# Kernel tuning notes

Hardware: AMD Instinct MI355X
Metric: run time of the kernel (lower is better)

## Reference

```python
import jax, jax.numpy as jnp
import numpy as np

VOCAB, EMBED, ZCH = 4096, 128, 256
B, H, W = 32, 16, 16


def setup_inputs() -> dict:
    key = jax.random.key(0)
    k1, k2, k3, k4 = jax.random.split(key, 4)
    z_e = jax.random.normal(k1, (B, ZCH, H, W), dtype=jnp.float32)
    pre_w = jax.random.normal(k2, (EMBED, ZCH), dtype=jnp.float32) * 0.02
    pre_b = jnp.zeros((EMBED,), dtype=jnp.float32)
    # codebook initialized uniform(-1/vocab, 1/vocab) like the torch module
    emb = jax.random.uniform(k3, (VOCAB, EMBED), dtype=jnp.float32,
                             minval=-1.0 / VOCAB, maxval=1.0 / VOCAB)
    post_w = jax.random.normal(k4, (ZCH, EMBED), dtype=jnp.float32) * 0.02
    post_b = jnp.zeros((ZCH,), dtype=jnp.float32)
    return {"z_e": z_e, "pre_w": pre_w, "pre_b": pre_b, "emb": emb,
            "post_w": post_w, "post_b": post_b}


def reference(z_e, pre_w, pre_b, emb, post_w, post_b):
    # pre_quant_conv: 1x1 conv == per-pixel linear, z_channels -> embed_dim
    z = jnp.einsum('bchw,ec->behw', z_e, pre_w) + pre_b[None, :, None, None]
    b, e, h, w = z.shape
    zf = z.transpose(0, 2, 3, 1).reshape(-1, e)                 # (b*h*w, e)
    # squared distance to all codebook vectors: |z|^2 + |c|^2 - 2 z.c
    dist = (jnp.sum(zf * zf, axis=1, keepdims=True)
            + jnp.sum(emb * emb, axis=1)
            - 2.0 * zf @ emb.T)                                  # (b*h*w, vocab)
    tokens = jnp.argmin(dist, axis=-1)                           # (b*h*w,)
    z_q = emb[tokens].reshape(b, h, w, e).transpose(0, 3, 1, 2)  # (b,e,h,w)
    # straight-through estimator
    dec_in = z + jax.lax.stop_gradient(z_q - z)
    # post_quant_conv: 1x1 conv embed_dim -> z_channels (decoder input)
    rec = jnp.einsum('behw,ce->bchw', dec_in, post_w) + post_b[None, :, None, None]
    return z, z_q, rec
```

## Files before the change

### kernel.cpp

```cpp
#include <hip/hip_runtime.h>
#include <hip/hip_bf16.h>
#include <cstdint>

#define NB   32
#define NC   256
#define NE   128
#define NS   256
#define NV   4096
#define NP   8192
#define NSPLIT 8

typedef unsigned short ushort_t;
typedef __attribute__((ext_vector_type(8))) short bf16x8;
typedef __attribute__((ext_vector_type(8))) unsigned short us8;
typedef __attribute__((ext_vector_type(4))) float f32x4;

__device__ __forceinline__ float bf2f(ushort_t u) {
    union { unsigned int i; float f; } x; x.i = ((unsigned int)u) << 16; return x.f;
}
__device__ __forceinline__ ushort_t f2bf(float f) {
    __hip_bfloat16 h = __float2bfloat16(f);
    ushort_t u; __builtin_memcpy(&u, &h, 2); return u;
}
__device__ __forceinline__ unsigned asu(float f) { unsigned u; __builtin_memcpy(&u,&f,4); return u; }
__device__ __forceinline__ float    asf(unsigned u) { float f; __builtin_memcpy(&f,&u,4); return f; }

__global__ __launch_bounds__(256) void pre_conv_pack(
    const float* __restrict__ z_e, const float* __restrict__ pre_w,
    const float* __restrict__ pre_b, const float* __restrict__ emb,
    float* __restrict__ out_z, ushort_t* __restrict__ Bpack,
    float* __restrict__ cnorm)
{
    __shared__ __align__(16) float wtile[16 * 256];
    __shared__ __align__(16) float part[4 * 16 * 64];

    const int t = threadIdx.x;

    if (blockIdx.x == 8) {
        const int v     = (blockIdx.y * 4 + blockIdx.z) * 32 + (t >> 3);
        const int chunk = t & 7;
        const float4* rp = (const float4*)(emb + (size_t)v * NE + chunk * 16);
        float4 x0 = rp[0], x1 = rp[1], x2 = rp[2], x3 = rp[3];
        float xs[16] = { x0.x, x0.y, x0.z, x0.w, x1.x, x1.y, x1.z, x1.w,
                         x2.x, x2.y, x2.z, x2.w, x3.x, x3.y, x3.z, x3.w };
        us8 h0, h1;
        float nn = 0.f;
#pragma unroll
        for (int j = 0; j < 8; j++) {
            nn = fmaf(xs[j], xs[j], nn);
            h0[j] = f2bf(xs[j]);
        }
#pragma unroll
        for (int j = 0; j < 8; j++) {
            nn = fmaf(xs[8 + j], xs[8 + j], nn);
            h1[j] = f2bf(xs[8 + j]);
        }
        nn += __shfl_xor(nn, 1);
        nn += __shfl_xor(nn, 2);
        nn += __shfl_xor(nn, 4);
        if (chunk == 0) cnorm[v] = 0.5f * nn;

        const int G  = v >> 4;
        const int ks = chunk >> 1;
        const int q0 = (chunk & 1) * 2;
        const int L0 = (v & 15) | (q0 << 4);
        const int L1 = (v & 15) | ((q0 + 1) << 4);
        *(us8*)(Bpack + ((size_t)G * 4 + ks) * 512 + L0 * 8) = h0;
        *(us8*)(Bpack + ((size_t)G * 4 + ks) * 512 + L1 * 8) = h1;
        return;
    }

    const int e0 = blockIdx.x * 16;
    const int b  = blockIdx.y;
    const int s0 = blockIdx.z * 64;

    for (int idx = t; idx < 16 * 256; idx += 256)
        wtile[idx] = pre_w[(e0 + (idx >> 8)) * 256 + (idx & 255)];
    __syncthreads();

    const int kq = t >> 6, sl = t & 63;
    float acc[16];
#pragma unroll
    for (int r = 0; r < 16; r++) acc[r] = 0.f;

    const float* zin = z_e + (size_t)(b * NC + kq * 64) * NS + s0 + sl;
    const int cb = kq * 64;
#pragma unroll 4
    for (int i = 0; i < 16; i++) {
        const int c = i * 4;
        float z0 = zin[(c + 0) * NS];
        float z1 = zin[(c + 1) * NS];
        float z2 = zin[(c + 2) * NS];
        float z3 = zin[(c + 3) * NS];
#pragma unroll
        for (int r = 0; r < 16; r++) {
            float4 w = *(const float4*)&wtile[r * 256 + cb + c];
            acc[r] = fmaf(z0, w.x, fmaf(z1, w.y, fmaf(z2, w.z, fmaf(z3, w.w, acc[r]))));
        }
    }
#pragma unroll
    for (int r = 0; r < 16; r++)
        part[(kq * 16 + r) * 64 + sl] = acc[r];
    __syncthreads();

    const int r4 = t >> 6, sl2 = t & 63;
#pragma unroll
    for (int j = 0; j < 4; j++) {
        const int r = j * 4 + r4;
        float v = pre_b[e0 + r]
                + part[(0 * 16 + r) * 64 + sl2]
                + part[(1 * 16 + r) * 64 + sl2]
                + part[(2 * 16 + r) * 64 + sl2]
                + part[(3 * 16 + r) * 64 + sl2];
        out_z[(size_t)(b * NE + e0 + r) * NS + s0 + sl2] = v;
    }
}

__global__ __launch_bounds__(256, 3) void score_mfma(
    const float* __restrict__ z, const ushort_t* __restrict__ Bpack,
    const float* __restrict__ cnorm, int* __restrict__ pidx4)
{
    __shared__ __align__(16) char smraw[37376];
    float* As  = (float*)smraw;
    float* r1  = (float*)smraw;
    float* r2  = (float*)(smraw + 16640);
    float* t4b = (float*)(smraw + 33280);

    const int t = threadIdx.x;
    const int wave = t >> 6, lane = t & 63;
    const int set = blockIdx.x;
    const int split = blockIdx.y;
    const int p0 = set * 64;
    const int b  = p0 >> 8;
    const int s0 = p0 & 255;

    for (int idx = t; idx < 64 * 128; idx += 256) {
        int k = idx >> 6, i = idx & 63;
        As[i * 132 + k] = z[(size_t)(b * NE + k) * NS + s0 + i];
    }
    __syncthreads();

    const int am = lane & 15, aq = lane >> 4;
    bf16x8 ah[4][4];
#pragma unroll
    for (int mt = 0; mt < 4; mt++)
#pragma unroll
        for (int ks = 0; ks < 4; ks++) {
            const unsigned* src = (const unsigned*)(As + (mt * 16 + am) * 132 + ks * 32 + aq * 8);
            union { unsigned u[4]; bf16x8 v; } pk;
#pragma unroll
            for (int pr = 0; pr < 4; pr++)
                pk.u[pr] = (src[2 * pr + 1] & 0xFFFF0000u) | (src[2 * pr] >> 16);
            ah[mt][ks] = pk.v;
        }
    __syncthreads();

    const int Gbase = split * 32 + wave * 8;
    float cn[8];
#pragma unroll
    for (int cgi = 0; cgi < 8; cgi++)
        cn[cgi] = cnorm[(Gbase + cgi) * 16 + am];

    float b1v[16], b2v[16];
#pragma unroll
    for (int i = 0; i < 16; i++) { b1v[i] = -1e30f; b2v[i] = -1e30f; }

    for (int cgi = 0; cgi < 8; cgi++) {
        const int G = Gbase + cgi;
        bf16x8 bh[4];
#pragma unroll
        for (int ks = 0; ks < 4; ks++)
            bh[ks] = *(const bf16x8*)(Bpack + ((size_t)G * 4 + ks) * 512 + lane * 8);

        f32x4 acc[4];
#pragma unroll
        for (int mt = 0; mt < 4; mt++) acc[mt] = (f32x4){0.f, 0.f, 0.f, 0.f};
#pragma unroll
        for (int ks = 0; ks < 4; ks++)
#pragma unroll
            for (int mt = 0; mt < 4; mt++)
                acc[mt] = __builtin_amdgcn_mfma_f32_16x16x32_bf16(ah[mt][ks], bh[ks], acc[mt], 0, 0, 0);

#pragma unroll
        for (int mt = 0; mt < 4; mt++)
#pragma unroll
            for (int reg = 0; reg < 4; reg++) {
                const int si = mt * 4 + reg;
                float sc = acc[mt][reg] - cn[cgi];
                float ev = asf((asu(sc) & ~7u) | (unsigned)cgi);
                b2v[si] = fmaxf(b2v[si], fminf(ev, b1v[si]));
                b1v[si] = fmaxf(b1v[si], ev);
            }
    }

    const int slot = wave * 16 + am;
#pragma unroll
    for (int mt = 0; mt < 4; mt++)
#pragma unroll
        for (int reg = 0; reg < 4; reg++) {
            int px = mt * 16 + aq * 4 + reg;
            r1[slot * 65 + px] = b1v[mt * 4 + reg];
            r2[slot * 65 + px] = b2v[mt * 4 + reg];
        }
    __syncthreads();

    {
        const int px = t >> 2, ch = t & 3;
        float t1 = -1e30f, t2 = -1e30f, t3 = -1e30f, t4 = -1e30f;
        for (int i = 0; i < 16; i++) {
            int sl = ch * 16 + i;
#pragma unroll
            for (int e = 0; e < 2; e++) {
                float raw = e ? r2[sl * 65 + px] : r1[sl * 65 + px];
                unsigned vb = asu(raw);
                float v = asf((vb & ~511u) | ((unsigned)sl << 3) | (vb & 7u));
                t4 = fmaxf(t4, fminf(v, t3));
                t3 = fmaxf(t3, fminf(v, t2));
                t2 = fmaxf(t2, fminf(v, t1));
                t1 = fmaxf(t1, v);
            }
        }
        float* dst = t4b + (px * 4 + ch) * 4;
        dst[0] = t1; dst[1] = t2; dst[2] = t3; dst[3] = t4;
    }
    __syncthreads();

    if (t < 64) {
        float u1 = -1e30f, u2 = -1e30f, u3 = -1e30f, u4 = -1e30f;
        for (int ch = 0; ch < 4; ch++) {
#pragma unroll
            for (int j = 0; j < 4; j++) {
                float v = t4b[(t * 4 + ch) * 4 + j];
                u4 = fmaxf(u4, fminf(v, u3));
                u3 = fmaxf(u3, fminf(v, u2));
                u2 = fmaxf(u2, fminf(v, u1));
                u1 = fmaxf(u1, v);
            }
        }
        const int p = p0 + t;
        float uu[4] = { u1, u2, u3, u4 };
#pragma unroll
        for (int j = 0; j < 4; j++) {
            unsigned bits = asu(uu[j]) & 511u;
            int w = (int)(bits >> 7), res = (int)((bits >> 3) & 15u), cg = (int)(bits & 7u);
            pidx4[((size_t)split * NP + p) * 4 + j] = split * 512 + (w * 8 + cg) * 16 + res;
        }
    }
}

__global__ __launch_bounds__(256) void rescore_gather(
    const float* __restrict__ z, const float* __restrict__ emb,
    const float* __restrict__ cnorm, const int* __restrict__ pidx4,
    float* __restrict__ out_zq)
{
    __shared__ __align__(16) float zl[16 * 132];
    __shared__ float bsl[16 * 16];
    __shared__ int   bil[16 * 16];
    __shared__ int   tok[16];

    const int t  = threadIdx.x;
    const int p0 = blockIdx.x * 16;
    const int b  = p0 >> 8;
    const int s0 = p0 & 255;

    for (int idx = t; idx < 16 * 128; idx += 256) {
        int k = idx >> 4, i = idx & 15;
        zl[i * 132 + k] = z[(size_t)(b * NE + k) * NS + s0 + i];
    }
    __syncthreads();

    const int il = t >> 4;
    const int cc = t & 15;
    const int p  = p0 + il;
    float bs = -1e30f; int bi = 0x7fffffff;
#pragma unroll
    for (int jj = 0; jj < 2; jj++) {
        int cand = cc * 2 + jj;
        int split = cand >> 2, slot = cand & 3;
        int idx = pidx4[((size_t)split * NP + p) * 4 + slot];
        const float* er = emb + (size_t)idx * NE;
        float d0 = 0.f, d1 = 0.f, d2 = 0.f, d3 = 0.f;
        for (int k = 0; k < NE; k += 4) {
            float4 e4 = *(const float4*)(er + k);
            d0 = fmaf(zl[il * 132 + k + 0], e4.x, d0);
            d1 = fmaf(zl[il * 132 + k + 1], e4.y, d1);
            d2 = fmaf(zl[il * 132 + k + 2], e4.z, d2);
            d3 = fmaf(zl[il * 132 + k + 3], e4.w, d3);
        }
        float sc = (d0 + d1) + (d2 + d3) - cnorm[idx];
        if (sc > bs || (sc == bs && idx < bi)) { bs = sc; bi = idx; }
    }
    bsl[il * 16 + cc] = bs;
    bil[il * 16 + cc] = bi;
    __syncthreads();

    if (t < 16) {
        float B = -1e30f; int I = 0x7fffffff;
        for (int c = 0; c < 16; c++) {
            float sc = bsl[t * 16 + c]; int ii = bil[t * 16 + c];
            if (sc > B || (sc == B && ii < I)) { B = sc; I = ii; }
        }
        tok[t] = I;
    }
    __syncthreads();

    for (int idx = t; idx < NE * 16; idx += 256) {
        int e = idx >> 4, i = idx & 15;
        out_zq[(size_t)(b * NE + e) * NS + s0 + i] = emb[(size_t)tok[i] * NE + e];
    }
}

__global__ __launch_bounds__(256) void post_conv(
    const float* __restrict__ zq, const float* __restrict__ post_w,
    const float* __restrict__ post_b, float* __restrict__ out_rec)
{
    __shared__ __align__(16) float wtile[16 * 128];
    __shared__ __align__(16) float part[4 * 16 * 64];

    const int t  = threadIdx.x;
    const int c0 = blockIdx.x * 16;
    const int b  = blockIdx.y;
    const int s0 = blockIdx.z * 64;

    for (int idx = t; idx < 16 * 128; idx += 256)
        wtile[idx] = post_w[(c0 + (idx >> 7)) * 128 + (idx & 127)];
    __syncthreads();

    const int kq = t >> 6, sl = t & 63;
    float acc[16];
#pragma unroll
    for (int r = 0; r < 16; r++) acc[r] = 0.f;

    const float* zin = zq + (size_t)(b * NE + kq * 32) * NS + s0 + sl;
    const int eb = kq * 32;
#pragma unroll 4
    for (int i = 0; i < 8; i++) {
        const int e = i * 4;
        float z0 = zin[(e + 0) * NS];
        float z1 = zin[(e + 1) * NS];
        float z2 = zin[(e + 2) * NS];
        float z3 = zin[(e + 3) * NS];
#pragma unroll
        for (int r = 0; r < 16; r++) {
            float4 w = *(const float4*)&wtile[r * 128 + eb + e];
            acc[r] = fmaf(z0, w.x, fmaf(z1, w.y, fmaf(z2, w.z, fmaf(z3, w.w, acc[r]))));
        }
    }
#pragma unroll
    for (int r = 0; r < 16; r++)
        part[(kq * 16 + r) * 64 + sl] = acc[r];
    __syncthreads();

    const int r4 = t >> 6, sl2 = t & 63;
#pragma unroll
    for (int j = 0; j < 4; j++) {
        const int r = j * 4 + r4;
        float v = post_b[c0 + r]
                + part[(0 * 16 + r) * 64 + sl2]
                + part[(1 * 16 + r) * 64 + sl2]
                + part[(2 * 16 + r) * 64 + sl2]
                + part[(3 * 16 + r) * 64 + sl2];
        out_rec[(size_t)(b * NC + c0 + r) * NS + s0 + sl2] = v;
    }
}

extern "C" void kernel_launch(void* const* d_in, const int* in_sizes, int n_in,
                              void* d_out, int out_size, void* d_ws, size_t ws_size,
                              hipStream_t stream)
{
    const float* z_e    = (const float*)d_in[0];
    const float* pre_w  = (const float*)d_in[1];
    const float* pre_b  = (const float*)d_in[2];
    const float* emb    = (const float*)d_in[3];
    const float* post_w = (const float*)d_in[4];
    const float* post_b = (const float*)d_in[5];

    float* out     = (float*)d_out;
    float* out_z   = out;
    float* out_zq  = out + 1048576;
    float* out_rec = out + 2097152;

    const size_t SZ_BPACK = (size_t)256 * 4 * 512 * 2;
    const size_t SZ_CNORM = (size_t)NV * 4;
    const size_t SZ_PIDX4 = (size_t)NSPLIT * NP * 4 * 4;
    const size_t NEED = SZ_BPACK + SZ_CNORM + SZ_PIDX4;
    char* scr = (ws_size >= NEED) ? (char*)d_ws : (char*)out_rec;
    ushort_t* Bpack = (ushort_t*)scr;
    float*    cnorm = (float*)(scr + SZ_BPACK);
    int*      pidx4 = (int*)(scr + SZ_BPACK + SZ_CNORM);

    pre_conv_pack <<<dim3(9, 32, 4),     256, 0, stream>>>(z_e, pre_w, pre_b, emb,
                                                           out_z, Bpack, cnorm);
    score_mfma    <<<dim3(128, NSPLIT),  256, 0, stream>>>(out_z, Bpack, cnorm, pidx4);
    rescore_gather<<<dim3(512),          256, 0, stream>>>(out_z, emb, cnorm, pidx4, out_zq);
    post_conv     <<<dim3(16, 32, 4),    256, 0, stream>>>(out_zq, post_w, post_b, out_rec);
}
```

Measured before the change: 155.7 us.

## Fuse scoring, rescoring, gather and post-conv into one MFMA kernel

Replaces the split score kernel, the rescore/gather kernel and the post-conv kernel with a single kernel. Each of 128 blocks scans the whole codebook for its 64 pixels, then rescores the top candidates in fp32 from shared memory, writes z_q, and computes the post-quant conv with bf16 MFMA using a post_w copy packed in the pre-conv kernel. The aim is to remove two launches, the candidate-index round trip through global memory and the separate fp32 post-conv pass. In exchange only 128 blocks run, each with a much longer serial loop, so much of the GPU may sit idle. The reconstruction output is now computed from bf16-rounded operands.

```diff
diff --git a/kernel.cpp b/kernel.cpp
--- a/kernel.cpp
+++ b/kernel.cpp
@@ -8,7 +8,6 @@
 #define NS   256
 #define NV   4096
 #define NP   8192
-#define NSPLIT 8
 
 typedef unsigned short ushort_t;
 typedef __attribute__((ext_vector_type(8))) short bf16x8;
@@ -25,11 +24,30 @@
 __device__ __forceinline__ unsigned asu(float f) { unsigned u; __builtin_memcpy(&u,&f,4); return u; }
 __device__ __forceinline__ float    asf(unsigned u) { float f; __builtin_memcpy(&f,&u,4); return f; }
 
+__device__ __forceinline__ void ins4(float v, float& t1, float& t2, float& t3, float& t4) {
+    t4 = fmaxf(t4, fminf(v, t3));
+    t3 = fmaxf(t3, fminf(v, t2));
+    t2 = fmaxf(t2, fminf(v, t1));
+    t1 = fmaxf(t1, v);
+}
+
+__device__ __forceinline__ bf16x8 pack8(const float* p) {
+    uint4 a = *(const uint4*)p;
+    uint4 c = *(const uint4*)(p + 4);
+    union { unsigned u[4]; bf16x8 v; } pk;
+    pk.u[0] = (a.y & 0xFFFF0000u) | (a.x >> 16);
+    pk.u[1] = (a.w & 0xFFFF0000u) | (a.z >> 16);
+    pk.u[2] = (c.y & 0xFFFF0000u) | (c.x >> 16);
+    pk.u[3] = (c.w & 0xFFFF0000u) | (c.z >> 16);
+    return pk.v;
+}
+
 __global__ __launch_bounds__(256) void pre_conv_pack(
     const float* __restrict__ z_e, const float* __restrict__ pre_w,
     const float* __restrict__ pre_b, const float* __restrict__ emb,
+    const float* __restrict__ post_w,
     float* __restrict__ out_z, ushort_t* __restrict__ Bpack,
-    float* __restrict__ cnorm)
+    ushort_t* __restrict__ Wpack, float* __restrict__ cnorm)
 {
     __shared__ __align__(16) float wtile[16 * 256];
     __shared__ __align__(16) float part[4 * 16 * 64];
@@ -39,36 +57,39 @@
     if (blockIdx.x == 8) {
         const int v     = (blockIdx.y * 4 + blockIdx.z) * 32 + (t >> 3);
         const int chunk = t & 7;
-        const float4* rp = (const float4*)(emb + (size_t)v * NE + chunk * 16);
+        const float* row = (v < NV) ? (emb + (size_t)v * NE)
+                                    : (post_w + (size_t)(v - NV) * NE);
+        const float4* rp = (const float4*)(row + chunk * 16);
         float4 x0 = rp[0], x1 = rp[1], x2 = rp[2], x3 = rp[3];
         float xs[16] = { x0.x, x0.y, x0.z, x0.w, x1.x, x1.y, x1.z, x1.w,
                          x2.x, x2.y, x2.z, x2.w, x3.x, x3.y, x3.z, x3.w };
         us8 h0, h1;
         float nn = 0.f;
 #pragma unroll
-        for (int j = 0; j < 8; j++) {
-            nn = fmaf(xs[j], xs[j], nn);
-            h0[j] = f2bf(xs[j]);
-        }
-#pragma unroll
-        for (int j = 0; j < 8; j++) {
-            nn = fmaf(xs[8 + j], xs[8 + j], nn);
-            h1[j] = f2bf(xs[8 + j]);
-        }
+        for (int j = 0; j < 8; j++) { nn = fmaf(xs[j], xs[j], nn); h0[j] = f2bf(xs[j]); }
+#pragma unroll
+        for (int j = 0; j < 8; j++) { nn = fmaf(xs[8+j], xs[8+j], nn); h1[j] = f2bf(xs[8+j]); }
         nn += __shfl_xor(nn, 1);
         nn += __shfl_xor(nn, 2);
         nn += __shfl_xor(nn, 4);
-        if (chunk == 0) cnorm[v] = 0.5f * nn;
-
-        const int G  = v >> 4;
+
         const int ks = chunk >> 1;
         const int q0 = (chunk & 1) * 2;
         const int L0 = (v & 15) | (q0 << 4);
         const int L1 = (v & 15) | ((q0 + 1) << 4);
-        *(us8*)(Bpack + ((size_t)G * 4 + ks) * 512 + L0 * 8) = h0;
-        *(us8*)(Bpack + ((size_t)G * 4 + ks) * 512 + L1 * 8) = h1;
+        if (v < NV) {
+            if (chunk == 0) cnorm[v] = 0.5f * nn;
+            const int G = v >> 4;
+            *(us8*)(Bpack + ((size_t)G * 4 + ks) * 512 + L0 * 8) = h0;
+            *(us8*)(Bpack + ((size_t)G * 4 + ks) * 512 + L1 * 8) = h1;
+        } else {
+            const int G = (v - NV) >> 4;
+            *(us8*)(Wpack + ((size_t)G * 4 + ks) * 512 + L0 * 8) = h0;
+            *(us8*)(Wpack + ((size_t)G * 4 + ks) * 512 + L1 * 8) = h1;
+        }
         return;
     }
+    if (blockIdx.y >= 32) return;
 
     const int e0 = blockIdx.x * 16;
     const int b  = blockIdx.y;
@@ -116,23 +137,28 @@
     }
 }
 
-__global__ __launch_bounds__(256, 3) void score_mfma(
+__global__ __launch_bounds__(256) void mega(
     const float* __restrict__ z, const ushort_t* __restrict__ Bpack,
-    const float* __restrict__ cnorm, int* __restrict__ pidx4)
+    const ushort_t* __restrict__ Wpack, const float* __restrict__ cnorm,
+    const float* __restrict__ emb, const float* __restrict__ post_b,
+    float* __restrict__ out_zq, float* __restrict__ out_rec)
 {
-    __shared__ __align__(16) char smraw[37376];
+    __shared__ __align__(16) char smraw[40960];
     float* As  = (float*)smraw;
     float* r1  = (float*)smraw;
     float* r2  = (float*)(smraw + 16640);
-    float* t4b = (float*)(smraw + 33280);
+    float* t4b = (float*)(smraw + 33792);
+    float* bsl = (float*)(smraw + 37888);
+    int*   bil = (int*)  (smraw + 38912);
+    int*   tok = (int*)  (smraw + 39936);
 
     const int t = threadIdx.x;
     const int wave = t >> 6, lane = t & 63;
     const int set = blockIdx.x;
-    const int split = blockIdx.y;
     const int p0 = set * 64;
     const int b  = p0 >> 8;
     const int s0 = p0 & 255;
+    const int am = lane & 15, aq = lane >> 4;
 
     for (int idx = t; idx < 64 * 128; idx += 256) {
         int k = idx >> 6, i = idx & 63;
@@ -140,37 +166,26 @@
     }
     __syncthreads();
 
-    const int am = lane & 15, aq = lane >> 4;
     bf16x8 ah[4][4];
 #pragma unroll
     for (int mt = 0; mt < 4; mt++)
 #pragma unroll
-        for (int ks = 0; ks < 4; ks++) {
-            const unsigned* src = (const unsigned*)(As + (mt * 16 + am) * 132 + ks * 32 + aq * 8);
-            union { unsigned u[4]; bf16x8 v; } pk;
-#pragma unroll
-            for (int pr = 0; pr < 4; pr++)
-                pk.u[pr] = (src[2 * pr + 1] & 0xFFFF0000u) | (src[2 * pr] >> 16);
-            ah[mt][ks] = pk.v;
-        }
-    __syncthreads();
-
-    const int Gbase = split * 32 + wave * 8;
-    float cn[8];
-#pragma unroll
-    for (int cgi = 0; cgi < 8; cgi++)
-        cn[cgi] = cnorm[(Gbase + cgi) * 16 + am];
-
+        for (int ks = 0; ks < 4; ks++)
+            ah[mt][ks] = pack8(As + (mt * 16 + am) * 132 + ks * 32 + aq * 8);
+    __syncthreads();
+
+    const int Gbase = wave * 64;
     float b1v[16], b2v[16];
 #pragma unroll
     for (int i = 0; i < 16; i++) { b1v[i] = -1e30f; b2v[i] = -1e30f; }
 
-    for (int cgi = 0; cgi < 8; cgi++) {
+    for (int cgi = 0; cgi < 64; cgi++) {
         const int G = Gbase + cgi;
         bf16x8 bh[4];
 #pragma unroll
         for (int ks = 0; ks < 4; ks++)
             bh[ks] = *(const bf16x8*)(Bpack + ((size_t)G * 4 + ks) * 512 + lane * 8);
+        const float cn = cnorm[G * 16 + am];
 
         f32x4 acc[4];
 #pragma unroll
@@ -186,8 +201,8 @@
 #pragma unroll
             for (int reg = 0; reg < 4; reg++) {
                 const int si = mt * 4 + reg;
-                float sc = acc[mt][reg] - cn[cgi];
-                float ev = asf((asu(sc) & ~7u) | (unsigned)cgi);
+                float sc = acc[mt][reg] - cn;
+                float ev = asf((asu(sc) & ~63u) | (unsigned)cgi);
                 b2v[si] = fmaxf(b2v[si], fminf(ev, b1v[si]));
                 b1v[si] = fmaxf(b1v[si], ev);
             }
@@ -213,11 +228,8 @@
             for (int e = 0; e < 2; e++) {
                 float raw = e ? r2[sl * 65 + px] : r1[sl * 65 + px];
                 unsigned vb = asu(raw);
-                float v = asf((vb & ~511u) | ((unsigned)sl << 3) | (vb & 7u));
-                t4 = fmaxf(t4, fminf(v, t3));
-                t3 = fmaxf(t3, fminf(v, t2));
-                t2 = fmaxf(t2, fminf(v, t1));
-                t1 = fmaxf(t1, v);
+                float v = asf((vb & ~4095u) | ((unsigned)sl << 6) | (vb & 63u));
+                ins4(v, t1, t2, t3, t4);
             }
         }
         float* dst = t4b + (px * 4 + ch) * 4;
@@ -225,142 +237,89 @@
     }
     __syncthreads();
 
+    for (int idx = t; idx < 64 * 128; idx += 256) {
+        int k = idx >> 6, i = idx & 63;
+        As[i * 132 + k] = z[(size_t)(b * NE + k) * NS + s0 + i];
+    }
+    __syncthreads();
+
+    {
+        const int px = t >> 2, ch = t & 3;
+        float best = -1e30f; int bi = 0x7fffffff;
+#pragma unroll
+        for (int j = 0; j < 4; j++) {
+            unsigned bits = asu(t4b[(px * 4 + ch) * 4 + j]) & 4095u;
+            int sl = (int)(bits >> 6), cgi = (int)(bits & 63u);
+            int code = (sl >> 4) * 1024 + cgi * 16 + (sl & 15);
+            const float* er = (const float*)(Bpack);
+            (void)er;
+            float d0 = 0.f, d1 = 0.f, d2 = 0.f, d3 = 0.f;
+            const float* cr = emb + (size_t)code * NE;
+            const float* zr = As + px * 132;
+            for (int k = 0; k < NE; k += 4) {
+                float4 e4 = *(const float4*)(cr + k);
+                d0 = fmaf(zr[k + 0], e4.x, d0);
+                d1 = fmaf(zr[k + 1], e4.y, d1);
+                d2 = fmaf(zr[k + 2], e4.z, d2);
+                d3 = fmaf(zr[k + 3], e4.w, d3);
+            }
+            float sc = (d0 + d1) + (d2 + d3) - cnorm[code];
+            if (sc > best || (sc == best && code < bi)) { best = sc; bi = code; }
+        }
+        bsl[px * 4 + ch] = best;
+        bil[px * 4 + ch] = bi;
+    }
+    __syncthreads();
+
     if (t < 64) {
-        float u1 = -1e30f, u2 = -1e30f, u3 = -1e30f, u4 = -1e30f;
-        for (int ch = 0; ch < 4; ch++) {
-#pragma unroll
-            for (int j = 0; j < 4; j++) {
-                float v = t4b[(t * 4 + ch) * 4 + j];
-                u4 = fmaxf(u4, fminf(v, u3));
-                u3 = fmaxf(u3, fminf(v, u2));
-                u2 = fmaxf(u2, fminf(v, u1));
-                u1 = fmaxf(u1, v);
-            }
-        }
-        const int p = p0 + t;
-        float uu[4] = { u1, u2, u3, u4 };
-#pragma unroll
-        for (int j = 0; j < 4; j++) {
-            unsigned bits = asu(uu[j]) & 511u;
-            int w = (int)(bits >> 7), res = (int)((bits >> 3) & 15u), cg = (int)(bits & 7u);
-            pidx4[((size_t)split * NP + p) * 4 + j] = split * 512 + (w * 8 + cg) * 16 + res;
-        }
-    }
-}
-
-__global__ __launch_bounds__(256) void rescore_gather(
-    const float* __restrict__ z, const float* __restrict__ emb,
-    const float* __restrict__ cnorm, const int* __restrict__ pidx4,
-    float* __restrict__ out_zq)
-{
-    __shared__ __align__(16) float zl[16 * 132];
-    __shared__ float bsl[16 * 16];
-    __shared__ int   bil[16 * 16];
-    __shared__ int   tok[16];
-
-    const int t  = threadIdx.x;
-    const int p0 = blockIdx.x * 16;
-    const int b  = p0 >> 8;
-    const int s0 = p0 & 255;
-
-    for (int idx = t; idx < 16 * 128; idx += 256) {
-        int k = idx >> 4, i = idx & 15;
-        zl[i * 132 + k] = z[(size_t)(b * NE + k) * NS + s0 + i];
-    }
-    __syncthreads();
-
-    const int il = t >> 4;
-    const int cc = t & 15;
-    const int p  = p0 + il;
-    float bs = -1e30f; int bi = 0x7fffffff;
-#pragma unroll
-    for (int jj = 0; jj < 2; jj++) {
-        int cand = cc * 2 + jj;
-        int split = cand >> 2, slot = cand & 3;
-        int idx = pidx4[((size_t)split * NP + p) * 4 + slot];
-        const float* er = emb + (size_t)idx * NE;
-        float d0 = 0.f, d1 = 0.f, d2 = 0.f, d3 = 0.f;
-        for (int k = 0; k < NE; k += 4) {
-            float4 e4 = *(const float4*)(er + k);
-            d0 = fmaf(zl[il * 132 + k + 0], e4.x, d0);
-            d1 = fmaf(zl[il * 132 + k + 1], e4.y, d1);
-            d2 = fmaf(zl[il * 132 + k + 2], e4.z, d2);
-            d3 = fmaf(zl[il * 132 + k + 3], e4.w, d3);
-        }
-        float sc = (d0 + d1) + (d2 + d3) - cnorm[idx];
-        if (sc > bs || (sc == bs && idx < bi)) { bs = sc; bi = idx; }
-    }
-    bsl[il * 16 + cc] = bs;
-    bil[il * 16 + cc] = bi;
-    __syncthreads();
-
-    if (t < 16) {
         float B = -1e30f; int I = 0x7fffffff;
-        for (int c = 0; c < 16; c++) {
-            float sc = bsl[t * 16 + c]; int ii = bil[t * 16 + c];
+#pragma unroll
+        for (int c = 0; c < 4; c++) {
+            float sc = bsl[t * 4 + c]; int ii = bil[t * 4 + c];
             if (sc > B || (sc == B && ii < I)) { B = sc; I = ii; }
         }
         tok[t] = I;
     }
     __syncthreads();
 
-    for (int idx = t; idx < NE * 16; idx += 256) {
-        int e = idx >> 4, i = idx & 15;
+    for (int idx = t; idx < NE * 64; idx += 256) {
+        int e = idx >> 6, i = idx & 63;
         out_zq[(size_t)(b * NE + e) * NS + s0 + i] = emb[(size_t)tok[i] * NE + e];
     }
-}
-
-__global__ __launch_bounds__(256) void post_conv(
-    const float* __restrict__ zq, const float* __restrict__ post_w,
-    const float* __restrict__ post_b, float* __restrict__ out_rec)
-{
-    __shared__ __align__(16) float wtile[16 * 128];
-    __shared__ __align__(16) float part[4 * 16 * 64];
-
-    const int t  = threadIdx.x;
-    const int c0 = blockIdx.x * 16;
-    const int b  = blockIdx.y;
-    const int s0 = blockIdx.z * 64;
-
-    for (int idx = t; idx < 16 * 128; idx += 256)
-        wtile[idx] = post_w[(c0 + (idx >> 7)) * 128 + (idx & 127)];
-    __syncthreads();
-
-    const int kq = t >> 6, sl = t & 63;
-    float acc[16];
-#pragma unroll
-    for (int r = 0; r < 16; r++) acc[r] = 0.f;
-
-    const float* zin = zq + (size_t)(b * NE + kq * 32) * NS + s0 + sl;
-    const int eb = kq * 32;
-#pragma unroll 4
-    for (int i = 0; i < 8; i++) {
-        const int e = i * 4;
-        float z0 = zin[(e + 0) * NS];
-        float z1 = zin[(e + 1) * NS];
-        float z2 = zin[(e + 2) * NS];
-        float z3 = zin[(e + 3) * NS];
-#pragma unroll
-        for (int r = 0; r < 16; r++) {
-            float4 w = *(const float4*)&wtile[r * 128 + eb + e];
-            acc[r] = fmaf(z0, w.x, fmaf(z1, w.y, fmaf(z2, w.z, fmaf(z3, w.w, acc[r]))));
-        }
-    }
-#pragma unroll
-    for (int r = 0; r < 16; r++)
-        part[(kq * 16 + r) * 64 + sl] = acc[r];
-    __syncthreads();
-
-    const int r4 = t >> 6, sl2 = t & 63;
-#pragma unroll
-    for (int j = 0; j < 4; j++) {
-        const int r = j * 4 + r4;
-        float v = post_b[c0 + r]
-                + part[(0 * 16 + r) * 64 + sl2]
-                + part[(1 * 16 + r) * 64 + sl2]
-                + part[(2 * 16 + r) * 64 + sl2]
-                + part[(3 * 16 + r) * 64 + sl2];
-        out_rec[(size_t)(b * NC + c0 + r) * NS + s0 + sl2] = v;
+
+    bf16x8 af[4][4];
+#pragma unroll
+    for (int mt = 0; mt < 4; mt++) {
+        const int tk = tok[mt * 16 + am];
+        const float* rp = emb + (size_t)tk * NE;
+#pragma unroll
+        for (int ks = 0; ks < 4; ks++)
+            af[mt][ks] = pack8(rp + ks * 32 + aq * 8);
+    }
+#pragma unroll
+    for (int g = 0; g < 4; g++) {
+        const int ng = wave * 4 + g;
+        const int c  = ng * 16 + am;
+        bf16x8 wb[4];
+#pragma unroll
+        for (int ks = 0; ks < 4; ks++)
+            wb[ks] = *(const bf16x8*)(Wpack + ((size_t)ng * 4 + ks) * 512 + lane * 8);
+
+        f32x4 d[4];
+#pragma unroll
+        for (int mt = 0; mt < 4; mt++) d[mt] = (f32x4){0.f, 0.f, 0.f, 0.f};
+#pragma unroll
+        for (int ks = 0; ks < 4; ks++)
+#pragma unroll
+            for (int mt = 0; mt < 4; mt++)
+                d[mt] = __builtin_amdgcn_mfma_f32_16x16x32_bf16(af[mt][ks], wb[ks], d[mt], 0, 0, 0);
+
+        const float pb = post_b[c];
+#pragma unroll
+        for (int mt = 0; mt < 4; mt++) {
+            float4 v = make_float4(d[mt][0] + pb, d[mt][1] + pb, d[mt][2] + pb, d[mt][3] + pb);
+            *(float4*)(out_rec + (size_t)(b * NC + c) * NS + s0 + mt * 16 + aq * 4) = v;
+        }
     }
 }
 
@@ -381,17 +340,16 @@
     float* out_rec = out + 2097152;
 
     const size_t SZ_BPACK = (size_t)256 * 4 * 512 * 2;
+    const size_t SZ_WPACK = (size_t)16 * 4 * 512 * 2;
     const size_t SZ_CNORM = (size_t)NV * 4;
-    const size_t SZ_PIDX4 = (size_t)NSPLIT * NP * 4 * 4;
-    const size_t NEED = SZ_BPACK + SZ_CNORM + SZ_PIDX4;
+    const size_t NEED = SZ_BPACK + SZ_WPACK + SZ_CNORM;
     char* scr = (ws_size >= NEED) ? (char*)d_ws : (char*)out_rec;
     ushort_t* Bpack = (ushort_t*)scr;
-    float*    cnorm = (float*)(scr + SZ_BPACK);
-    int*      pidx4 = (int*)(scr + SZ_BPACK + SZ_CNORM);
-
-    pre_conv_pack <<<dim3(9, 32, 4),     256, 0, stream>>>(z_e, pre_w, pre_b, emb,
-                                                           out_z, Bpack, cnorm);
-    score_mfma    <<<dim3(128, NSPLIT),  256, 0, stream>>>(out_z, Bpack, cnorm, pidx4);
-    rescore_gather<<<dim3(512),          256, 0, stream>>>(out_z, emb, cnorm, pidx4, out_zq);
-    post_conv     <<<dim3(16, 32, 4),    256, 0, stream>>>(out_zq, post_w, post_b, out_rec);
-}
+    ushort_t* Wpack = (ushort_t*)(scr + SZ_BPACK);
+    float*    cnorm = (float*)(scr + SZ_BPACK + SZ_WPACK);
+
+    pre_conv_pack<<<dim3(9, 34, 4), 256, 0, stream>>>(
+        z_e, pre_w, pre_b, emb, post_w, out_z, Bpack, Wpack, cnorm);
+    mega<<<dim3(128), 256, 0, stream>>>(
+        out_z, Bpack, Wpack, cnorm, emb, post_b, out_zq, out_rec);
+}
```

After: 170.0 us. +9.2%, slower.
